# Kernel tuning notes

Hardware: AMD Instinct MI355X
Metric: run time of the kernel (lower is better)

The kernel has to match this reference:

```python
import jax, jax.numpy as jnp
import numpy as np
import math

H = 1024  # hidden_dim
NH = 16   # num_heads
HD = H // NH  # head_dim = 64
B, S, C = 2, 2048, 256  # batch, seq_len, cond_len
EPS = 1e-5


def layernorm(x, g, b):
    m = jnp.mean(x, axis=-1, keepdims=True)
    v = jnp.var(x, axis=-1, keepdims=True)
    return (x - m) * jax.lax.rsqrt(v + EPS) * g + b


def apply_rope(x, freqs):
    # x: [b, s, h, d], freqs broadcastable to [b, s, h, d//2]
    cos, sin = jnp.cos(freqs), jnp.sin(freqs)
    x1, x2 = jnp.split(x, 2, axis=-1)
    return jnp.concatenate([x1 * cos - x2 * sin, x2 * cos + x1 * sin], axis=-1)


def setup_inputs() -> dict:
    key = jax.random.key(0)
    ks = jax.random.split(key, 16)
    sc = 0.02
    x = jax.random.normal(ks[0], (B, S, H), jnp.float32)
    # rope freqs: positions * inv_freq over half head dim
    inv_freq = 1.0 / (10000.0 ** (jnp.arange(HD // 2, dtype=jnp.float32) / (HD // 2)))
    rope_freqs = (jnp.arange(S, dtype=jnp.float32)[:, None] * inv_freq[None, :]).reshape(S, 1, HD // 2)
    # causal additive mask [1,1,S,S]
    causal = jnp.tril(jnp.ones((S, S), dtype=bool))
    attention_mask = jnp.where(causal, 0.0, -1e9).astype(jnp.float32)[None, None]
    conditioning = jax.random.normal(ks[1], (B, C, H), jnp.float32)
    conditioning_mask = jnp.zeros((B, 1, 1, C), jnp.float32)
    params = dict(
        ln1_g=jnp.ones((H,)), ln1_b=jnp.zeros((H,)),
        ln2_g=jnp.ones((H,)), ln2_b=jnp.zeros((H,)),
        lnc_g=jnp.ones((H,)), lnc_b=jnp.zeros((H,)),
        w_qkv=jax.random.normal(ks[2], (H, 3 * H)) * sc,
        w_out=jax.random.normal(ks[3], (H, H)) * sc, b_out=jnp.zeros((H,)),
        w_cq=jax.random.normal(ks[4], (H, H)) * sc,
        w_ckv=jax.random.normal(ks[5], (H, 2 * H)) * sc,
        w_cout=jax.random.normal(ks[6], (H, H)) * sc, b_cout=jnp.zeros((H,)),
        w_ff1=jax.random.normal(ks[7], (H, 4 * H)) * sc, b_ff1=jnp.zeros((4 * H,)),
        w_ff2=jax.random.normal(ks[8], (4 * H, H)) * sc, b_ff2=jnp.zeros((H,)),
    )
    return dict(x=x, rope_freqs=rope_freqs, attention_mask=attention_mask,
                conditioning=conditioning, conditioning_mask=conditioning_mask, **params)


def reference(x, rope_freqs, attention_mask, conditioning, conditioning_mask,
              ln1_g, ln1_b, ln2_g, ln2_b, lnc_g, lnc_b,
              w_qkv, w_out, b_out, w_cq, w_ckv, w_cout, b_cout,
              w_ff1, b_ff1, w_ff2, b_ff2):
    scale = 1.0 / math.sqrt(HD)
    # --- causal self-attention ---
    residual = x
    h = layernorm(x, ln1_g, ln1_b)
    qkv = h @ w_qkv  # [b,s,3H]
    q, k, v = jnp.split(qkv, 3, axis=-1)
    q = q.reshape(B, S, NH, HD)
    k = k.reshape(B, S, NH, HD)
    v = v.reshape(B, S, NH, HD)
    q = apply_rope(q, rope_freqs)
    k = apply_rope(k, rope_freqs)
    scores = jnp.einsum('bqhd,bkhd->bhqk', q, k) * scale + attention_mask
    attn = jax.nn.softmax(scores, axis=-1)
    out = jnp.einsum('bhqk,bkhd->bqhd', attn, v).reshape(B, S, H)
    x = residual + out @ w_out + b_out
    # --- cross-attention ---
    residual = x
    h = layernorm(x, lnc_g, lnc_b)
    q = (h @ w_cq).reshape(B, S, NH, HD)
    kv = conditioning @ w_ckv
    k, v = jnp.split(kv, 2, axis=-1)
    k = k.reshape(B, C, NH, HD)
    v = v.reshape(B, C, NH, HD)
    scores = jnp.einsum('bqhd,bkhd->bhqk', q, k) * scale + conditioning_mask
    attn = jax.nn.softmax(scores, axis=-1)
    out = jnp.einsum('bhqk,bkhd->bqhd', attn, v).reshape(B, S, H)
    x = residual + out @ w_cout + b_cout
    # --- FFN ---
    residual = x
    h = layernorm(x, ln2_g, ln2_b)
    h = jax.nn.gelu(h @ w_ff1 + b_ff1, approximate=False)
    x = residual + h @ w_ff2 + b_ff2
    return x
```

## Files before the change

kernel.cpp:

```cpp
#include <hip/hip_runtime.h>

#define HDIM   1024
#define NHEADS 16
#define HEADD  64
#define BATCH  2
#define SEQ    2048
#define CLEN   256
#define NROWS  (BATCH*SEQ)
#define SCALE  0.125f
#define LOG2E  1.44269504088896f

typedef __bf16 bf16x8 __attribute__((ext_vector_type(8)));
typedef float  f32x4  __attribute__((ext_vector_type(4)));

__device__ __forceinline__ unsigned short f2bf(float f) {
  union { __bf16 b; unsigned short u; } x;
  x.b = (__bf16)f;
  return x.u;
}
__device__ __forceinline__ float bf2f(unsigned short u) {
  union { unsigned int u; float f; } x; x.u = ((unsigned int)u) << 16;
  return x.f;
}

__device__ __forceinline__ void gl2lds16(const unsigned short* g, unsigned short* l) {
  __builtin_amdgcn_global_load_lds(
      (const __attribute__((address_space(1))) unsigned int*)g,
      (__attribute__((address_space(3))) unsigned int*)l, 16, 0, 0);
}

__global__ __launch_bounds__(256)
void cast_transpose64(const float* __restrict__ in, unsigned short* __restrict__ out,
                      int K, int N) {
  __shared__ float t[64][68];
  const int kb = blockIdx.y * 64, nb = blockIdx.x * 64;
  const int tid = threadIdx.x;
  const int r = tid >> 4, c = (tid & 15) * 4;
#pragma unroll
  for (int i = 0; i < 4; ++i) {
    float4 v = *(const float4*)(in + (size_t)(kb + r + i * 16) * N + nb + c);
    t[r + i * 16][c]     = v.x;
    t[r + i * 16][c + 1] = v.y;
    t[r + i * 16][c + 2] = v.z;
    t[r + i * 16][c + 3] = v.w;
  }
  __syncthreads();
  const int nr = tid >> 3, kc = (tid & 7) * 8;
#pragma unroll
  for (int i = 0; i < 2; ++i) {
    unsigned short us[8];
#pragma unroll
    for (int j = 0; j < 8; ++j) us[j] = f2bf(t[kc + j][nr + i * 32]);
    *(uint4*)(out + (size_t)(nb + nr + i * 32) * K + kb + kc) = *(uint4*)us;
  }
}

__global__ void cast_kernel8(const float* __restrict__ in, unsigned short* __restrict__ out, int n8) {
  int i = blockIdx.x * 256 + threadIdx.x;
  if (i < n8) {
    float4 a = ((const float4*)in)[2 * i], b = ((const float4*)in)[2 * i + 1];
    unsigned short us[8] = { f2bf(a.x), f2bf(a.y), f2bf(a.z), f2bf(a.w),
                             f2bf(b.x), f2bf(b.y), f2bf(b.z), f2bf(b.w) };
    ((uint4*)out)[i] = *(uint4*)us;
  }
}

__global__ __launch_bounds__(256)
void vtrans_kernel(const unsigned short* __restrict__ in, int str, int voff, int rows,
                   unsigned short* __restrict__ out) {
  __shared__ unsigned short t[64][72];
  const int h = blockIdx.y & (NHEADS - 1), b = blockIdx.y >> 4;
  const int s0 = blockIdx.x * 64;
  const int tid = threadIdx.x;
  const int r = tid >> 2, c = (tid & 3) * 16;
  const unsigned short* src = in + (size_t)(b * rows + s0 + r) * str + voff + h * 64 + c;
  *(uint4*)(&t[r][c])     = *(const uint4*)(src);
  *(uint4*)(&t[r][c + 8]) = *(const uint4*)(src + 8);
  __syncthreads();
  const int d = tid >> 2, sc = (tid & 3) * 16;
  unsigned short tmp[16];
#pragma unroll
  for (int i = 0; i < 16; ++i) tmp[i] = t[sc + i][d];
  unsigned short* dst = out + ((size_t)(b * NHEADS + h) * 64 + d) * rows + s0 + sc;
  *(uint4*)(dst)     = *(uint4*)(tmp);
  *(uint4*)(dst + 8) = *(uint4*)(tmp + 8);
}

__global__ __launch_bounds__(256)
void layernorm_kernel(const float* __restrict__ x, const float* __restrict__ g,
                      const float* __restrict__ b, unsigned short* __restrict__ out) {
  int row = blockIdx.x;
  const float4 v = ((const float4*)(x + (size_t)row * HDIM))[threadIdx.x];
  float s  = v.x + v.y + v.z + v.w;
  float sq = v.x*v.x + v.y*v.y + v.z*v.z + v.w*v.w;
  for (int o = 32; o; o >>= 1) { s += __shfl_xor(s, o); sq += __shfl_xor(sq, o); }
  __shared__ float rs[4], rq[4];
  int wave = threadIdx.x >> 6;
  if ((threadIdx.x & 63) == 0) { rs[wave] = s; rq[wave] = sq; }
  __syncthreads();
  s  = rs[0] + rs[1] + rs[2] + rs[3];
  sq = rq[0] + rq[1] + rq[2] + rq[3];
  float mean = s * (1.f/HDIM);
  float var  = sq * (1.f/HDIM) - mean*mean;
  float rstd = rsqrtf(var + 1e-5f);
  float4 gg = ((const float4*)g)[threadIdx.x];
  float4 bb = ((const float4*)b)[threadIdx.x];
  ushort4 o;
  o.x = f2bf((v.x - mean) * rstd * gg.x + bb.x);
  o.y = f2bf((v.y - mean) * rstd * gg.y + bb.y);
  o.z = f2bf((v.z - mean) * rstd * gg.z + bb.z);
  o.w = f2bf((v.w - mean) * rstd * gg.w + bb.w);
  ((ushort4*)(out + (size_t)row * HDIM))[threadIdx.x] = o;
}

template<int TBM, int TBN, bool BIAS, bool RES, bool GELU_, bool OUTBF>
__global__ __launch_bounds__(256)
void gemm_bt(const unsigned short* __restrict__ A, const unsigned short* __restrict__ Bt,
             const float* __restrict__ bias, const float* __restrict__ res,
             void* __restrict__ out, int M, int N, int K) {
  constexpr int MR = TBM / 32;
  constexpr int NR = TBN / 32;
  __shared__ unsigned short Al[2][TBM * 64];
  __shared__ unsigned short Bl[2][TBN * 64];
  const int tid  = threadIdx.x;
  const int wave = tid >> 6, lane = tid & 63;
  const int wr = wave >> 1, wc = wave & 1;
  const int nwg = gridDim.x * gridDim.y;
  int lin = blockIdx.y * gridDim.x + blockIdx.x;
  lin = (lin & 7) * (nwg >> 3) + (lin >> 3);
  const int m0 = (lin / gridDim.x) * TBM, n0 = (lin % gridDim.x) * TBN;
  const int lrow = lane & 15, hi = lane >> 4;
  const int rx = lrow & 7;

  f32x4 acc[MR][NR] = {};

  const int trow = tid >> 3, pslot = tid & 7;
  const int lcol = (pslot ^ (trow & 7)) * 8;
  const unsigned short* ga = A  + (size_t)(m0 + trow) * K + lcol;
  const unsigned short* gb = Bt + (size_t)(n0 + trow) * K + lcol;
  const int ldst = trow * 64 + pslot * 8;
  const int nt = K >> 6;

#pragma unroll
  for (int i = 0; i < MR; ++i)
    gl2lds16(ga + (size_t)i * 32 * K, Al[0] + ldst + i * 32 * 64);
#pragma unroll
  for (int i = 0; i < NR; ++i)
    gl2lds16(gb + (size_t)i * 32 * K, Bl[0] + ldst + i * 32 * 64);
  __syncthreads();

  int cur = 0;
  for (int t = 0; t < nt; ++t) {
    if (t + 1 < nt) {
      const int k1 = (t + 1) << 6;
#pragma unroll
      for (int i = 0; i < MR; ++i)
        gl2lds16(ga + (size_t)i * 32 * K + k1, Al[cur ^ 1] + ldst + i * 32 * 64);
#pragma unroll
      for (int i = 0; i < NR; ++i)
        gl2lds16(gb + (size_t)i * 32 * K + k1, Bl[cur ^ 1] + ldst + i * 32 * 64);
    }
#pragma unroll
    for (int kk = 0; kk < 2; ++kk) {
      const int cslot = ((kk << 2) | hi);
      const int coff  = (cslot ^ rx) * 8;
      bf16x8 af[MR], bfr[NR];
#pragma unroll
      for (int m = 0; m < MR; ++m)
        af[m] = *(const bf16x8*)(Al[cur] + (wr*(TBM/2) + m*16 + lrow) * 64 + coff);
#pragma unroll
      for (int n = 0; n < NR; ++n)
        bfr[n] = *(const bf16x8*)(Bl[cur] + (wc*(TBN/2) + n*16 + lrow) * 64 + coff);
#pragma unroll
      for (int m = 0; m < MR; ++m)
#pragma unroll
        for (int n = 0; n < NR; ++n)
          acc[m][n] = __builtin_amdgcn_mfma_f32_16x16x32_bf16(af[m], bfr[n], acc[m][n], 0, 0, 0);
    }
    __syncthreads();
    cur ^= 1;
  }

#pragma unroll
  for (int m = 0; m < MR; ++m)
#pragma unroll
    for (int n = 0; n < NR; ++n)
#pragma unroll
      for (int r = 0; r < 4; ++r) {
        int row = m0 + wr*(TBM/2) + m*16 + hi * 4 + r;
        int col = n0 + wc*(TBN/2) + n*16 + lrow;
        float v = acc[m][n][r];
        if (BIAS)  v += bias[col];
        if (GELU_) v = 0.5f * v * (1.0f + erff(v * 0.70710678118654752f));
        if (RES)   v += res[(size_t)row * N + col];
        if (OUTBF) ((unsigned short*)out)[(size_t)row * N + col] = f2bf(v);
        else       ((float*)out)[(size_t)row * N + col] = v;
      }
}

__global__ void rope_kernel(unsigned short* __restrict__ qkv, const float* __restrict__ freqs) {
  int idx = blockIdx.x * 256 + threadIdx.x;
  int d = idx & 31;
  int h = (idx >> 5) & 15;
  int row = idx >> 9;
  int s = row & (SEQ - 1);
  float f = freqs[s * 32 + d];
  float sn, cs;
  sincosf(f, &sn, &cs);
  size_t base = (size_t)row * 3072 + h * 64 + d;
  float x1 = bf2f(qkv[base]), x2 = bf2f(qkv[base + 32]);
  qkv[base]      = f2bf(x1 * cs - x2 * sn);
  qkv[base + 32] = f2bf(x2 * cs + x1 * sn);
  float y1 = bf2f(qkv[base + 1024]), y2 = bf2f(qkv[base + 1024 + 32]);
  qkv[base + 1024]      = f2bf(y1 * cs - y2 * sn);
  qkv[base + 1024 + 32] = f2bf(y2 * cs + y1 * sn);
}

__global__ __launch_bounds__(512)
void flash_attn_causal8(const unsigned short* __restrict__ qp, int qstr,
                        const unsigned short* __restrict__ kp, int kstr,
                        const unsigned short* __restrict__ vt,
                        unsigned short* __restrict__ outp) {
  __shared__ unsigned short Kl[2][64 * 64];
  __shared__ unsigned short Vl[2][64 * 64];
  __shared__ unsigned short Pl[8][16][72];

  const int h = blockIdx.y & (NHEADS - 1), b = blockIdx.y >> 4;
  const int tid = threadIdx.x;
  const int wave = tid >> 6, lane = tid & 63;
  const int grp = wave >> 2, w4 = wave & 3;
  const int lo = lane & 15, hi = lane >> 4;
  const int NQB = SEQ / 64;
  const float SC2 = SCALE * LOG2E;
  float* mb = (float*)&Pl[0][0][0];

  const unsigned short* vbase = vt + (size_t)(b * NHEADS + h) * 64 * SEQ;
  const int g256 = tid & 255;
  const int trow = g256 >> 3, pslot = g256 & 7;
  const int lcol = (pslot ^ (trow & 7)) * 8;
  const int ldst = g256 * 8;
  const int x7 = lo & 7;
  const int c0 = (hi ^ x7) * 8, c1 = ((hi + 4) ^ x7) * 8;

  for (int pass = 0; pass < 2; ++pass) {
    const int qblk = pass == 0 ? (int)blockIdx.x : NQB - 1 - (int)blockIdx.x;
    const int q0 = qblk * 64;
    const int qw = q0 + w4 * 16;

    bf16x8 qf[2];
    {
      const unsigned short* qb = qp + (size_t)(b * SEQ + qw + lo) * qstr + h * 64 + hi * 8;
      qf[0] = *(const bf16x8*)(qb);
      qf[1] = *(const bf16x8*)(qb + 32);
    }

    f32x4 o_acc[4] = {};
    float mrow[4], lrow[4];
#pragma unroll
    for (int r = 0; r < 4; ++r) { mrow[r] = -1e30f; lrow[r] = 0.f; }

    const int T = qblk + 1;
    const int iters = (T + 1) >> 1;
    for (int it = 0; it < iters; ++it) {
      const int t = 2 * it + grp;
      const bool act = t < T;
      const int j0 = t * 64;
      if (act) {
        const unsigned short* ks = kp + (size_t)(b * SEQ + j0 + trow) * kstr + h * 64 + lcol;
        const unsigned short* vs = vbase + (size_t)trow * SEQ + j0 + lcol;
        gl2lds16(ks, Kl[grp] + ldst);
        gl2lds16(ks + (size_t)32 * kstr, Kl[grp] + ldst + 32 * 64);
        gl2lds16(vs, Vl[grp] + ldst);
        gl2lds16(vs + (size_t)32 * SEQ, Vl[grp] + ldst + 32 * 64);
      }
      __syncthreads();
      if (act) {
        const unsigned short* Kc = Kl[grp];
        const unsigned short* Vc = Vl[grp];
        f32x4 s[4] = {};
#pragma unroll
        for (int n = 0; n < 4; ++n) {
          bf16x8 b0 = *(const bf16x8*)(Kc + (n * 16 + lo) * 64 + c0);
          bf16x8 b1 = *(const bf16x8*)(Kc + (n * 16 + lo) * 64 + c1);
          s[n] = __builtin_amdgcn_mfma_f32_16x16x32_bf16(qf[0], b0, s[n], 0, 0, 0);
          s[n] = __builtin_amdgcn_mfma_f32_16x16x32_bf16(qf[1], b1, s[n], 0, 0, 0);
        }
        if (t == T - 1) {
#pragma unroll
          for (int n = 0; n < 4; ++n)
#pragma unroll
            for (int r = 0; r < 4; ++r)
              if (j0 + n * 16 + lo > qw + hi * 4 + r) s[n][r] = -1e30f;
        }
        float pr[4][4];
#pragma unroll
        for (int r = 0; r < 4; ++r) {
          float mx = -1e30f;
#pragma unroll
          for (int n = 0; n < 4; ++n) {
            float v = s[n][r] * SC2;
            s[n][r] = v;
            mx = fmaxf(mx, v);
          }
          mx = fmaxf(mx, __shfl_xor(mx, 1));
          mx = fmaxf(mx, __shfl_xor(mx, 2));
          mx = fmaxf(mx, __shfl_xor(mx, 4));
          mx = fmaxf(mx, __shfl_xor(mx, 8));
          const float mnew = fmaxf(mrow[r], mx);
          const float corr = exp2f(mrow[r] - mnew);
          mrow[r] = mnew;
          float ls = 0.f;
#pragma unroll
          for (int n = 0; n < 4; ++n) {
            float p = exp2f(s[n][r] - mnew);
            pr[n][r] = p;
            ls += p;
          }
          ls += __shfl_xor(ls, 1);
          ls += __shfl_xor(ls, 2);
          ls += __shfl_xor(ls, 4);
          ls += __shfl_xor(ls, 8);
          lrow[r] = lrow[r] * corr + ls;
#pragma unroll
          for (int n2 = 0; n2 < 4; ++n2) o_acc[n2][r] *= corr;
        }
#pragma unroll
        for (int n = 0; n < 4; ++n)
#pragma unroll
          for (int r = 0; r < 4; ++r)
            Pl[wave][hi * 4 + r][n * 16 + lo] = f2bf(pr[n][r]);

        bf16x8 pa0 = *(const bf16x8*)(&Pl[wave][lo][hi * 8]);
        bf16x8 pa1 = *(const bf16x8*)(&Pl[wave][lo][32 + hi * 8]);
#pragma unroll
        for (int n = 0; n < 4; ++n) {
          bf16x8 vb0 = *(const bf16x8*)(Vc + (n * 16 + lo) * 64 + c0);
          bf16x8 vb1 = *(const bf16x8*)(Vc + (n * 16 + lo) * 64 + c1);
          o_acc[n] = __builtin_amdgcn_mfma_f32_16x16x32_bf16(pa0, vb0, o_acc[n], 0, 0, 0);
          o_acc[n] = __builtin_amdgcn_mfma_f32_16x16x32_bf16(pa1, vb1, o_acc[n], 0, 0, 0);
        }
      }
      __syncthreads();
    }

    unsigned short* ob = outp + (size_t)(b * SEQ + qw) * HDIM + h * 64;
#pragma unroll
    for (int half = 0; half < 2; ++half) {
      __syncthreads();
      if (grp == 1) {
        float* dst = mb + (w4 * 64 + lane) * 13;
#pragma unroll
        for (int rr = 0; rr < 2; ++rr) {
          int r = half * 2 + rr;
          dst[rr * 6]     = mrow[r];
          dst[rr * 6 + 1] = lrow[r];
#pragma unroll
          for (int n = 0; n < 4; ++n) dst[rr * 6 + 2 + n] = o_acc[n][r];
        }
      }
      __syncthreads();
      if (grp == 0) {
        const float* s1 = mb + (w4 * 64 + lane) * 13;
#pragma unroll
        for (int rr = 0; rr < 2; ++rr) {
          int r = half * 2 + rr;
          float m1 = s1[rr * 6], l1 = s1[rr * 6 + 1];
          float M  = fmaxf(mrow[r], m1);
          float c0f = exp2f(mrow[r] - M), c1f = exp2f(m1 - M);
          float inv = 1.f / (lrow[r] * c0f + l1 * c1f);
#pragma unroll
          for (int n = 0; n < 4; ++n) {
            float o = o_acc[n][r] * c0f + s1[rr * 6 + 2 + n] * c1f;
            ob[(size_t)(hi * 4 + r) * HDIM + n * 16 + lo] = f2bf(o * inv);
          }
        }
      }
    }
    __syncthreads();
  }
}

__global__ __launch_bounds__(256)
void flash_attn_cross(const unsigned short* __restrict__ qp, int qstr,
                      const unsigned short* __restrict__ kp, int kstr,
                      const unsigned short* __restrict__ vt,
                      int kvrows, const float* __restrict__ mask,
                      unsigned short* __restrict__ outp) {
  __shared__ unsigned short Kl[2][64 * 64];
  __shared__ unsigned short Vl[2][64 * 64];
  __shared__ unsigned short Pl[4][16][72];

  const int h = blockIdx.y & (NHEADS - 1), b = blockIdx.y >> 4;
  const int tid = threadIdx.x;
  const int wave = tid >> 6, lane = tid & 63;
  const int lo = lane & 15, hi = lane >> 4;
  const float SC2 = SCALE * LOG2E;

  const unsigned short* vbase = vt + (size_t)(b * NHEADS + h) * 64 * kvrows;
  const int trow = tid >> 3, pslot = tid & 7;
  const int lcol = (pslot ^ (trow & 7)) * 8;
  const int ldst = tid * 8;
  const int x7 = lo & 7;
  const int c0 = (hi ^ x7) * 8, c1 = ((hi + 4) ^ x7) * 8;

  const int qw = blockIdx.x * 64 + wave * 16;

  bf16x8 qf[2];
  {
    const unsigned short* qb = qp + (size_t)(b * SEQ + qw + lo) * qstr + h * 64 + hi * 8;
    qf[0] = *(const bf16x8*)(qb);
    qf[1] = *(const bf16x8*)(qb + 32);
  }

  f32x4 o_acc[4] = {};
  float mrow[4], lrow[4];
#pragma unroll
  for (int r = 0; r < 4; ++r) { mrow[r] = -1e30f; lrow[r] = 0.f; }

  const int T = kvrows / 64;
  {
    const unsigned short* ks = kp + (size_t)(b * kvrows + trow) * kstr + h * 64 + lcol;
    const unsigned short* vs = vbase + (size_t)trow * kvrows + lcol;
    gl2lds16(ks, Kl[0] + ldst);
    gl2lds16(ks + (size_t)32 * kstr, Kl[0] + ldst + 32 * 64);
    gl2lds16(vs, Vl[0] + ldst);
    gl2lds16(vs + (size_t)32 * kvrows, Vl[0] + ldst + 32 * 64);
  }
  __syncthreads();

  int cur = 0;
  for (int t = 0; t < T; ++t) {
    if (t + 1 < T) {
      const int j1 = (t + 1) * 64;
      const unsigned short* ks = kp + (size_t)(b * kvrows + j1 + trow) * kstr + h * 64 + lcol;
      const unsigned short* vs = vbase + (size_t)trow * kvrows + j1 + lcol;
      gl2lds16(ks, Kl[cur ^ 1] + ldst);
      gl2lds16(ks + (size_t)32 * kstr, Kl[cur ^ 1] + ldst + 32 * 64);
      gl2lds16(vs, Vl[cur ^ 1] + ldst);
      gl2lds16(vs + (size_t)32 * kvrows, Vl[cur ^ 1] + ldst + 32 * 64);
    }
    const unsigned short* Kc = Kl[cur];
    const unsigned short* Vc = Vl[cur];
    const int j0 = t * 64;

    f32x4 s[4] = {};
#pragma unroll
    for (int n = 0; n < 4; ++n) {
      bf16x8 b0 = *(const bf16x8*)(Kc + (n * 16 + lo) * 64 + c0);
      bf16x8 b1 = *(const bf16x8*)(Kc + (n * 16 + lo) * 64 + c1);
      s[n] = __builtin_amdgcn_mfma_f32_16x16x32_bf16(qf[0], b0, s[n], 0, 0, 0);
      s[n] = __builtin_amdgcn_mfma_f32_16x16x32_bf16(qf[1], b1, s[n], 0, 0, 0);
    }

    float mk2[4];
#pragma unroll
    for (int n = 0; n < 4; ++n) mk2[n] = mask[b * kvrows + j0 + n * 16 + lo] * LOG2E;

    float pr[4][4];
#pragma unroll
    for (int r = 0; r < 4; ++r) {
      float mx = -1e30f;
#pragma unroll
      for (int n = 0; n < 4; ++n) {
        float v = s[n][r] * SC2 + mk2[n];
        s[n][r] = v;
        mx = fmaxf(mx, v);
      }
      mx = fmaxf(mx, __shfl_xor(mx, 1));
      mx = fmaxf(mx, __shfl_xor(mx, 2));
      mx = fmaxf(mx, __shfl_xor(mx, 4));
      mx = fmaxf(mx, __shfl_xor(mx, 8));
      const float mnew = fmaxf(mrow[r], mx);
      const float corr = exp2f(mrow[r] - mnew);
      mrow[r] = mnew;
      float ls = 0.f;
#pragma unroll
      for (int n = 0; n < 4; ++n) {
        float p = exp2f(s[n][r] - mnew);
        pr[n][r] = p;
        ls += p;
      }
      ls += __shfl_xor(ls, 1);
      ls += __shfl_xor(ls, 2);
      ls += __shfl_xor(ls, 4);
      ls += __shfl_xor(ls, 8);
      lrow[r] = lrow[r] * corr + ls;
#pragma unroll
      for (int n2 = 0; n2 < 4; ++n2) o_acc[n2][r] *= corr;
    }

#pragma unroll
    for (int n = 0; n < 4; ++n)
#pragma unroll
      for (int r = 0; r < 4; ++r)
        Pl[wave][hi * 4 + r][n * 16 + lo] = f2bf(pr[n][r]);

    bf16x8 pa0 = *(const bf16x8*)(&Pl[wave][lo][hi * 8]);
    bf16x8 pa1 = *(const bf16x8*)(&Pl[wave][lo][32 + hi * 8]);
#pragma unroll
    for (int n = 0; n < 4; ++n) {
      bf16x8 vb0 = *(const bf16x8*)(Vc + (n * 16 + lo) * 64 + c0);
      bf16x8 vb1 = *(const bf16x8*)(Vc + (n * 16 + lo) * 64 + c1);
      o_acc[n] = __builtin_amdgcn_mfma_f32_16x16x32_bf16(pa0, vb0, o_acc[n], 0, 0, 0);
      o_acc[n] = __builtin_amdgcn_mfma_f32_16x16x32_bf16(pa1, vb1, o_acc[n], 0, 0, 0);
    }
    __syncthreads();
    cur ^= 1;
  }

  unsigned short* ob = outp + (size_t)(b * SEQ + qw) * HDIM + h * 64;
#pragma unroll
  for (int r = 0; r < 4; ++r) {
    const float inv = 1.f / lrow[r];
#pragma unroll
    for (int n = 0; n < 4; ++n)
      ob[(size_t)(hi * 4 + r) * HDIM + n * 16 + lo] = f2bf(o_acc[n][r] * inv);
  }
}

extern "C" void kernel_launch(void* const* d_in, const int* in_sizes, int n_in,
                              void* d_out, int out_size, void* d_ws, size_t ws_size,
                              hipStream_t stream) {
  const float* x      = (const float*)d_in[0];
  const float* rfreq  = (const float*)d_in[1];
  const float* cond   = (const float*)d_in[3];
  const float* cmask  = (const float*)d_in[4];
  const float* ln1_g  = (const float*)d_in[5];
  const float* ln1_b  = (const float*)d_in[6];
  const float* ln2_g  = (const float*)d_in[7];
  const float* ln2_b  = (const float*)d_in[8];
  const float* lnc_g  = (const float*)d_in[9];
  const float* lnc_b  = (const float*)d_in[10];
  const float* w_qkv  = (const float*)d_in[11];
  const float* w_out  = (const float*)d_in[12];
  const float* b_out  = (const float*)d_in[13];
  const float* w_cq   = (const float*)d_in[14];
  const float* w_ckv  = (const float*)d_in[15];
  const float* w_cout = (const float*)d_in[16];
  const float* b_cout = (const float*)d_in[17];
  const float* w_ff1  = (const float*)d_in[18];
  const float* b_ff1  = (const float*)d_in[19];
  const float* w_ff2  = (const float*)d_in[20];
  const float* b_ff2  = (const float*)d_in[21];

  char* ws = (char*)d_ws;
  size_t off = 0;
  auto alloc = [&](size_t bytes) { size_t r = off; off += (bytes + 255) & ~(size_t)255; return r; };
  unsigned short* wt_qkv  = (unsigned short*)(ws + alloc((size_t)3072*1024*2));
  unsigned short* wt_out  = (unsigned short*)(ws + alloc((size_t)1024*1024*2));
  unsigned short* wt_cq   = (unsigned short*)(ws + alloc((size_t)1024*1024*2));
  unsigned short* wt_ckv  = (unsigned short*)(ws + alloc((size_t)2048*1024*2));
  unsigned short* wt_cout = (unsigned short*)(ws + alloc((size_t)1024*1024*2));
  unsigned short* wt_ff1  = (unsigned short*)(ws + alloc((size_t)4096*1024*2));
  unsigned short* wt_ff2  = (unsigned short*)(ws + alloc((size_t)1024*4096*2));
  unsigned short* condb   = (unsigned short*)(ws + alloc((size_t)512*1024*2));
  unsigned short* hbuf    = (unsigned short*)(ws + alloc((size_t)NROWS*1024*2));
  unsigned short* big     = (unsigned short*)(ws + alloc((size_t)NROWS*4096*2));
  unsigned short* attnb   = (unsigned short*)(ws + alloc((size_t)NROWS*1024*2));
  float*          x1      = (float*)(ws + alloc((size_t)NROWS*1024*4));
  unsigned short* kvc     = (unsigned short*)(ws + alloc((size_t)512*2048*2));
  unsigned short* vts     = (unsigned short*)(ws + alloc((size_t)BATCH*NHEADS*64*SEQ*2));
  unsigned short* vtc     = (unsigned short*)(ws + alloc((size_t)BATCH*NHEADS*64*CLEN*2));
  float*          outf    = (float*)d_out;

  cast_transpose64<<<dim3(48, 16), 256, 0, stream>>>(w_qkv,  wt_qkv,  1024, 3072);
  cast_transpose64<<<dim3(16, 16), 256, 0, stream>>>(w_out,  wt_out,  1024, 1024);
  cast_transpose64<<<dim3(16, 16), 256, 0, stream>>>(w_cq,   wt_cq,   1024, 1024);
  cast_transpose64<<<dim3(32, 16), 256, 0, stream>>>(w_ckv,  wt_ckv,  1024, 2048);
  cast_transpose64<<<dim3(16, 16), 256, 0, stream>>>(w_cout, wt_cout, 1024, 1024);
  cast_transpose64<<<dim3(64, 16), 256, 0, stream>>>(w_ff1,  wt_ff1,  1024, 4096);
  cast_transpose64<<<dim3(16, 64), 256, 0, stream>>>(w_ff2,  wt_ff2,  4096, 1024);
  cast_kernel8<<<(512*1024/8 + 255)/256, 256, 0, stream>>>(cond, condb, 512*1024/8);

  layernorm_kernel<<<NROWS, 256, 0, stream>>>(x, ln1_g, ln1_b, hbuf);
  gemm_bt<128,128,false,false,false,true><<<dim3(3072/128, NROWS/128), 256, 0, stream>>>(
      hbuf, wt_qkv, nullptr, nullptr, big, NROWS, 3072, 1024);
  rope_kernel<<<(NROWS*NHEADS*32)/256, 256, 0, stream>>>(big, rfreq);
  vtrans_kernel<<<dim3(SEQ/64, BATCH*NHEADS), 256, 0, stream>>>(big, 3072, 2048, SEQ, vts);
  flash_attn_causal8<<<dim3(SEQ/64/2, BATCH*NHEADS), 512, 0, stream>>>(
      big, 3072, big + 1024, 3072, vts, attnb);
  gemm_bt<128,64,true,true,false,false><<<dim3(1024/64, NROWS/128), 256, 0, stream>>>(
      attnb, wt_out, b_out, x, x1, NROWS, 1024, 1024);

  layernorm_kernel<<<NROWS, 256, 0, stream>>>(x1, lnc_g, lnc_b, hbuf);
  gemm_bt<128,64,false,false,false,true><<<dim3(1024/64, NROWS/128), 256, 0, stream>>>(
      hbuf, wt_cq, nullptr, nullptr, big, NROWS, 1024, 1024);
  gemm_bt<64,64,false,false,false,true><<<dim3(2048/64, 512/64), 256, 0, stream>>>(
      condb, wt_ckv, nullptr, nullptr, kvc, 512, 2048, 1024);
  vtrans_kernel<<<dim3(CLEN/64, BATCH*NHEADS), 256, 0, stream>>>(kvc, 2048, 1024, CLEN, vtc);
  flash_attn_cross<<<dim3(SEQ/64, BATCH*NHEADS), 256, 0, stream>>>(
      big, 1024, kvc, 2048, vtc, CLEN, cmask, attnb);
  gemm_bt<128,64,true,true,false,false><<<dim3(1024/64, NROWS/128), 256, 0, stream>>>(
      attnb, wt_cout, b_cout, x1, outf, NROWS, 1024, 1024);

  layernorm_kernel<<<NROWS, 256, 0, stream>>>(outf, ln2_g, ln2_b, hbuf);
  gemm_bt<128,128,true,false,true,true><<<dim3(4096/128, NROWS/128), 256, 0, stream>>>(
      hbuf, wt_ff1, b_ff1, nullptr, big, NROWS, 4096, 1024);
  gemm_bt<128,64,true,true,false,false><<<dim3(1024/64, NROWS/128), 256, 0, stream>>>(
      big, wt_ff2, b_ff2, outf, outf, NROWS, 1024, 4096);
}
```

Measured before the change: 373.8 us.

## Add lazy softmax rescaling, fold scale into Q, and remap blocks for locality

```diff
diff --git a/kernel.cpp b/kernel.cpp
--- a/kernel.cpp
+++ b/kernel.cpp
@@ -225,7 +225,11 @@
   __shared__ unsigned short Vl[2][64 * 64];
   __shared__ unsigned short Pl[8][16][72];
 
-  const int h = blockIdx.y & (NHEADS - 1), b = blockIdx.y >> 4;
+  const int id = blockIdx.y * gridDim.x + blockIdx.x;
+  const int bh = (id & 7) * 4 + ((id >> 3) & 3);
+  const int qpair = id >> 5;
+  const int h = bh & (NHEADS - 1), b = bh >> 4;
+
   const int tid = threadIdx.x;
   const int wave = tid >> 6, lane = tid & 63;
   const int grp = wave >> 2, w4 = wave & 3;
@@ -243,7 +247,7 @@
   const int c0 = (hi ^ x7) * 8, c1 = ((hi + 4) ^ x7) * 8;
 
   for (int pass = 0; pass < 2; ++pass) {
-    const int qblk = pass == 0 ? (int)blockIdx.x : NQB - 1 - (int)blockIdx.x;
+    const int qblk = pass == 0 ? qpair : NQB - 1 - qpair;
     const int q0 = qblk * 64;
     const int qw = q0 + w4 * 16;
 
@@ -252,6 +256,11 @@
       const unsigned short* qb = qp + (size_t)(b * SEQ + qw + lo) * qstr + h * 64 + hi * 8;
       qf[0] = *(const bf16x8*)(qb);
       qf[1] = *(const bf16x8*)(qb + 32);
+#pragma unroll
+      for (int j = 0; j < 8; ++j) {
+        qf[0][j] = (__bf16)((float)qf[0][j] * SC2);
+        qf[1][j] = (__bf16)((float)qf[1][j] * SC2);
+      }
     }
 
     f32x4 o_acc[4] = {};
@@ -292,37 +301,56 @@
             for (int r = 0; r < 4; ++r)
               if (j0 + n * 16 + lo > qw + hi * 4 + r) s[n][r] = -1e30f;
         }
+        float mx[4];
+#pragma unroll
+        for (int r = 0; r < 4; ++r) {
+          float m1 = fmaxf(fmaxf(s[0][r], s[1][r]), fmaxf(s[2][r], s[3][r]));
+          m1 = fmaxf(m1, __shfl_xor(m1, 1));
+          m1 = fmaxf(m1, __shfl_xor(m1, 2));
+          m1 = fmaxf(m1, __shfl_xor(m1, 4));
+          m1 = fmaxf(m1, __shfl_xor(m1, 8));
+          mx[r] = m1;
+        }
         float pr[4][4];
-#pragma unroll
-        for (int r = 0; r < 4; ++r) {
-          float mx = -1e30f;
-#pragma unroll
-          for (int n = 0; n < 4; ++n) {
-            float v = s[n][r] * SC2;
-            s[n][r] = v;
-            mx = fmaxf(mx, v);
+        const bool grow = (mx[0] > mrow[0] + 8.f) || (mx[1] > mrow[1] + 8.f) ||
+                          (mx[2] > mrow[2] + 8.f) || (mx[3] > mrow[3] + 8.f);
+        if (__any(grow)) {
+#pragma unroll
+          for (int r = 0; r < 4; ++r) {
+            const float mnew = fmaxf(mrow[r], mx[r]);
+            const float corr = exp2f(mrow[r] - mnew);
+            mrow[r] = mnew;
+            float ls = 0.f;
+#pragma unroll
+            for (int n = 0; n < 4; ++n) {
+              float p = exp2f(s[n][r] - mnew);
+              pr[n][r] = p;
+              ls += p;
+            }
+            ls += __shfl_xor(ls, 1);
+            ls += __shfl_xor(ls, 2);
+            ls += __shfl_xor(ls, 4);
+            ls += __shfl_xor(ls, 8);
+            lrow[r] = lrow[r] * corr + ls;
+#pragma unroll
+            for (int n2 = 0; n2 < 4; ++n2) o_acc[n2][r] *= corr;
           }
-          mx = fmaxf(mx, __shfl_xor(mx, 1));
-          mx = fmaxf(mx, __shfl_xor(mx, 2));
-          mx = fmaxf(mx, __shfl_xor(mx, 4));
-          mx = fmaxf(mx, __shfl_xor(mx, 8));
-          const float mnew = fmaxf(mrow[r], mx);
-          const float corr = exp2f(mrow[r] - mnew);
-          mrow[r] = mnew;
-          float ls = 0.f;
-#pragma unroll
-          for (int n = 0; n < 4; ++n) {
-            float p = exp2f(s[n][r] - mnew);
-            pr[n][r] = p;
-            ls += p;
+        } else {
+#pragma unroll
+          for (int r = 0; r < 4; ++r) {
+            float ls = 0.f;
+#pragma unroll
+            for (int n = 0; n < 4; ++n) {
+              float p = exp2f(s[n][r] - mrow[r]);
+              pr[n][r] = p;
+              ls += p;
+            }
+            ls += __shfl_xor(ls, 1);
+            ls += __shfl_xor(ls, 2);
+            ls += __shfl_xor(ls, 4);
+            ls += __shfl_xor(ls, 8);
+            lrow[r] += ls;
           }
-          ls += __shfl_xor(ls, 1);
-          ls += __shfl_xor(ls, 2);
-          ls += __shfl_xor(ls, 4);
-          ls += __shfl_xor(ls, 8);
-          lrow[r] = lrow[r] * corr + ls;
-#pragma unroll
-          for (int n2 = 0; n2 < 4; ++n2) o_acc[n2][r] *= corr;
         }
 #pragma unroll
         for (int n = 0; n < 4; ++n)
@@ -390,7 +418,11 @@
   __shared__ unsigned short Vl[2][64 * 64];
   __shared__ unsigned short Pl[4][16][72];
 
-  const int h = blockIdx.y & (NHEADS - 1), b = blockIdx.y >> 4;
+  const int id = blockIdx.y * gridDim.x + blockIdx.x;
+  const int bh = (id & 7) * 4 + ((id >> 3) & 3);
+  const int qblk = id >> 5;
+  const int h = bh & (NHEADS - 1), b = bh >> 4;
+
   const int tid = threadIdx.x;
   const int wave = tid >> 6, lane = tid & 63;
   const int lo = lane & 15, hi = lane >> 4;
@@ -403,13 +435,18 @@
   const int x7 = lo & 7;
   const int c0 = (hi ^ x7) * 8, c1 = ((hi + 4) ^ x7) * 8;
 
-  const int qw = blockIdx.x * 64 + wave * 16;
+  const int qw = qblk * 64 + wave * 16;
 
   bf16x8 qf[2];
   {
     const unsigned short* qb = qp + (size_t)(b * SEQ + qw + lo) * qstr + h * 64 + hi * 8;
     qf[0] = *(const bf16x8*)(qb);
     qf[1] = *(const bf16x8*)(qb + 32);
+#pragma unroll
+    for (int j = 0; j < 8; ++j) {
+      qf[0][j] = (__bf16)((float)qf[0][j] * SC2);
+      qf[1][j] = (__bf16)((float)qf[1][j] * SC2);
+    }
   }
 
   f32x4 o_acc[4] = {};
@@ -456,37 +493,62 @@
 #pragma unroll
     for (int n = 0; n < 4; ++n) mk2[n] = mask[b * kvrows + j0 + n * 16 + lo] * LOG2E;
 
+    float mx[4];
+#pragma unroll
+    for (int r = 0; r < 4; ++r) {
+      float m1 = -1e30f;
+#pragma unroll
+      for (int n = 0; n < 4; ++n) {
+        float v = s[n][r] + mk2[n];
+        s[n][r] = v;
+        m1 = fmaxf(m1, v);
+      }
+      m1 = fmaxf(m1, __shfl_xor(m1, 1));
+      m1 = fmaxf(m1, __shfl_xor(m1, 2));
+      m1 = fmaxf(m1, __shfl_xor(m1, 4));
+      m1 = fmaxf(m1, __shfl_xor(m1, 8));
+      mx[r] = m1;
+    }
     float pr[4][4];
-#pragma unroll
-    for (int r = 0; r < 4; ++r) {
-      float mx = -1e30f;
-#pragma unroll
-      for (int n = 0; n < 4; ++n) {
-        float v = s[n][r] * SC2 + mk2[n];
-        s[n][r] = v;
-        mx = fmaxf(mx, v);
-      }
-      mx = fmaxf(mx, __shfl_xor(mx, 1));
-      mx = fmaxf(mx, __shfl_xor(mx, 2));
-      mx = fmaxf(mx, __shfl_xor(mx, 4));
-      mx = fmaxf(mx, __shfl_xor(mx, 8));
-      const float mnew = fmaxf(mrow[r], mx);
-      const float corr = exp2f(mrow[r] - mnew);
-      mrow[r] = mnew;
-      float ls = 0.f;
-#pragma unroll
-      for (int n = 0; n < 4; ++n) {
-        float p = exp2f(s[n][r] - mnew);
-        pr[n][r] = p;
-        ls += p;
-      }
-      ls += __shfl_xor(ls, 1);
-      ls += __shfl_xor(ls, 2);
-      ls += __shfl_xor(ls, 4);
-      ls += __shfl_xor(ls, 8);
-      lrow[r] = lrow[r] * corr + ls;
-#pragma unroll
-      for (int n2 = 0; n2 < 4; ++n2) o_acc[n2][r] *= corr;
+    const bool grow = (mx[0] > mrow[0] + 8.f) || (mx[1] > mrow[1] + 8.f) ||
+                      (mx[2] > mrow[2] + 8.f) || (mx[3] > mrow[3] + 8.f);
+    if (__any(grow)) {
+#pragma unroll
+      for (int r = 0; r < 4; ++r) {
+        const float mnew = fmaxf(mrow[r], mx[r]);
+        const float corr = exp2f(mrow[r] - mnew);
+        mrow[r] = mnew;
+        float ls = 0.f;
+#pragma unroll
+        for (int n = 0; n < 4; ++n) {
+          float p = exp2f(s[n][r] - mnew);
+          pr[n][r] = p;
+          ls += p;
+        }
+        ls += __shfl_xor(ls, 1);
+        ls += __shfl_xor(ls, 2);
+        ls += __shfl_xor(ls, 4);
+        ls += __shfl_xor(ls, 8);
+        lrow[r] = lrow[r] * corr + ls;
+#pragma unroll
+        for (int n2 = 0; n2 < 4; ++n2) o_acc[n2][r] *= corr;
+      }
+    } else {
+#pragma unroll
+      for (int r = 0; r < 4; ++r) {
+        float ls = 0.f;
+#pragma unroll
+        for (int n = 0; n < 4; ++n) {
+          float p = exp2f(s[n][r] - mrow[r]);
+          pr[n][r] = p;
+          ls += p;
+        }
+        ls += __shfl_xor(ls, 1);
+        ls += __shfl_xor(ls, 2);
+        ls += __shfl_xor(ls, 4);
+        ls += __shfl_xor(ls, 8);
+        lrow[r] += ls;
+      }
     }
 
 #pragma unroll
```

After: 389.9 us. +4.3%, slower.
